# Kernel tuning notes

Measured on AMD Instinct MI355X. Metric: run time of the kernel, lower is better.

Reference implementation:

```python
import jax, jax.numpy as jnp
import numpy as np

D_K = 128
SCALER = np.sqrt(D_K).astype(np.float32)

def setup_inputs() -> dict:
    key = jax.random.key(0)
    kq, kk, kv = jax.random.split(key, 3)
    B, L, D = 16, 2048, D_K
    q = jax.random.normal(kq, (B, L, D), dtype=jnp.float32)
    k = jax.random.normal(kk, (B, L, D), dtype=jnp.float32)
    v = jax.random.normal(kv, (B, L, D), dtype=jnp.float32)
    return {"q": q, "k": k, "v": v}

def reference(q, k, v):
    # score[b, i, j] = q[b, i, :] . k[b, j, :] / sqrt(d_k)
    score = jnp.einsum('bid,bjd->bij', q, k) / SCALER
    attn = jax.nn.softmax(score, axis=-1)
    # output[b, i, :] = sum_j attn[b, i, j] * v[b, j, :]
    return jnp.einsum('bij,bjd->bid', attn, v)
```

## Files before the change

### kernel.cpp

```cpp
#include <hip/hip_runtime.h>
#include <stdint.h>


typedef short bf16x8 __attribute__((ext_vector_type(8)));
typedef float f32x4 __attribute__((ext_vector_type(4)));
typedef unsigned int u32;
typedef unsigned short u16;

#define L_SEQ  2048
#define D_HEAD 128
#define NIT    32
#define TSZ    (16u * 2048u * 128u * 2u)

__device__ __forceinline__ unsigned pk2(float lo, float hi) {
    union { float f; unsigned u; } a, b;
    a.f = lo; b.f = hi;
    return __builtin_amdgcn_perm(b.u + 0x8000u, a.u + 0x8000u, 0x07060302u);
}
__device__ __forceinline__ float ex2(float x) { return __builtin_amdgcn_exp2f(x); }
__device__ __forceinline__ void gl_lds16(const u16* g, u16* l) {
    __builtin_amdgcn_global_load_lds(
        (const __attribute__((address_space(1))) u32*)g,
        (__attribute__((address_space(3))) u32*)l, 16, 0, 0);
}

__global__ __launch_bounds__(256, 4)
void prepass(const float* __restrict__ K, const float* __restrict__ V,
             u16* __restrict__ kb, u16* __restrict__ vt) {
    const int id = blockIdx.x, t = threadIdx.x;
    if (id < 512) {
        const float* src = K + (size_t)id * 64 * 128;
        u16*        dst = kb + (size_t)id * 64 * 128;
        const int r = t >> 2;
        #pragma unroll
        for (int i = 0; i < 4; ++i) {
            int gp = (t & 3) * 4 + i;
            int gs = gp ^ (r & 7);
            const float* s = src + r * 128 + gs * 8;
            float4 x0 = *(const float4*)s, x1 = *(const float4*)(s + 4);
            uint4 w;
            w.x = pk2(x0.x, x0.y); w.y = pk2(x0.z, x0.w);
            w.z = pk2(x1.x, x1.y); w.w = pk2(x1.z, x1.w);
            *(uint4*)(dst + r * 128 + gp * 8) = w;
        }
    } else {
        __shared__ float vl[64 * 132];
        const int bid = id - 512;
        const float* src = V + (size_t)bid * 64 * 128;
        {
            int r = t >> 2, c0 = (t & 3) * 32;
            #pragma unroll
            for (int j = 0; j < 8; ++j)
                *(float4*)(&vl[r * 132 + c0 + j * 4]) =
                    *(const float4*)(src + r * 128 + c0 + j * 4);
        }
        __syncthreads();
        u16* dst = vt + (size_t)bid * 8192;
        const int d = t >> 1;
        #pragma unroll
        for (int i = 0; i < 4; ++i) {
            int gp = (t & 1) * 4 + i;
            int kvb = (gp ^ (d & 7)) * 8;
            float p[8];
            #pragma unroll
            for (int j = 0; j < 8; ++j) p[j] = vl[(kvb + j) * 132 + d];
            uint4 w;
            w.x = pk2(p[0], p[1]); w.y = pk2(p[2], p[3]);
            w.z = pk2(p[4], p[5]); w.w = pk2(p[6], p[7]);
            *(uint4*)(dst + d * 64 + gp * 8) = w;
        }
    }
}

__global__ __launch_bounds__(256, 1)
void attn_fwd(const float* __restrict__ Qg, const u16* __restrict__ kb,
              const u16* __restrict__ vt, float* __restrict__ Og) {
    __shared__ __align__(16) char smem[51200];
    const int tid = threadIdx.x;
    const int wv = tid >> 6, lane = tid & 63;
    const int c = lane & 15, qd = lane >> 4, cx = c & 7;
    const int b = blockIdx.x & 15, qblk = blockIdx.x >> 4;

    const float* Qp = Qg + (size_t)b * L_SEQ * D_HEAD;
    const u16*   Kp = kb + (size_t)b * L_SEQ * D_HEAD;
    const u16*   Vp = vt + (size_t)b * 32 * 8192;
    u16* Kl = (u16*)smem;
    u16* Vl = (u16*)(smem + 16384);
    u16* Pl = (u16*)(smem + 32768) + wv * 2304;

    const int so = wv * 2048 + lane * 8;

    #pragma unroll
    for (int i = 0; i < 4; ++i) {
        gl_lds16(Kp + so + i * 512, Kl + so + i * 512);
        gl_lds16(Vp + so + i * 512, Vl + so + i * 512);
    }

    const float QS = 1.4426950408889634f / 11.313708498984761f;
    bf16x8 qf[2][4];
    #pragma unroll
    for (int s = 0; s < 2; ++s) {
        const float* qrow = Qp + (size_t)(qblk * 128 + wv * 32 + s * 16 + c) * 128 + qd * 8;
        #pragma unroll
        for (int kt = 0; kt < 4; ++kt) {
            float4 x0 = *(const float4*)(qrow + kt * 32);
            float4 x1 = *(const float4*)(qrow + kt * 32 + 4);
            union { unsigned u[4]; bf16x8 v; } tt;
            tt.u[0] = pk2(x0.x * QS, x0.y * QS);
            tt.u[1] = pk2(x0.z * QS, x0.w * QS);
            tt.u[2] = pk2(x1.x * QS, x1.y * QS);
            tt.u[3] = pk2(x1.z * QS, x1.w * QS);
            qf[s][kt] = tt.v;
        }
    }

    f32x4 acc[2][8];
    #pragma unroll
    for (int s = 0; s < 2; ++s)
        #pragma unroll
        for (int dt = 0; dt < 8; ++dt) acc[s][dt] = (f32x4){0.f, 0.f, 0.f, 0.f};
    float lrun[2] = {0.f, 0.f};

    __syncthreads();

    for (int it = 0; it < NIT; ++it) {
        f32x4 st[4][2];
        #pragma unroll
        for (int v = 0; v < 4; ++v) {
            st[v][0] = (f32x4){0.f, 0.f, 0.f, 0.f};
            st[v][1] = (f32x4){0.f, 0.f, 0.f, 0.f};
        }
        #pragma unroll
        for (int kt = 0; kt < 4; ++kt) {
            const int g = ((kt * 4 + qd) ^ cx) * 8;
            #pragma unroll
            for (int v = 0; v < 4; ++v) {
                bf16x8 a = *(const bf16x8*)(Kl + (v * 16 + c) * 128 + g);
                st[v][0] = __builtin_amdgcn_mfma_f32_16x16x32_bf16(a, qf[0][kt], st[v][0], 0, 0, 0);
                st[v][1] = __builtin_amdgcn_mfma_f32_16x16x32_bf16(a, qf[1][kt], st[v][1], 0, 0, 0);
            }
        }
        __syncthreads();

        if (it + 1 < NIT) {
            const u16* kg = Kp + (size_t)(it + 1) * 8192 + so;
            #pragma unroll
            for (int i = 0; i < 4; ++i) gl_lds16(kg + i * 512, Kl + so + i * 512);
        }

        #pragma unroll
        for (int s = 0; s < 2; ++s) {
            float lsum = 0.f;
            #pragma unroll
            for (int v = 0; v < 4; ++v) {
                float p0 = ex2(st[v][s].x), p1 = ex2(st[v][s].y);
                float p2 = ex2(st[v][s].z), p3 = ex2(st[v][s].w);
                lsum += (p0 + p1) + (p2 + p3);
                uint2 w; w.x = pk2(p0, p1); w.y = pk2(p2, p3);
                *(uint2*)(Pl + (s * 16 + c) * 72 + v * 16 + qd * 4) = w;
            }
            lrun[s] += lsum;
        }
        bf16x8 pf[2][2];
        #pragma unroll
        for (int h = 0; h < 2; ++h)
            #pragma unroll
            for (int s = 0; s < 2; ++s)
                pf[h][s] = *(const bf16x8*)(Pl + (s * 16 + c) * 72 + h * 32 + qd * 8);

        #pragma unroll
        for (int dt = 0; dt < 8; ++dt) {
            #pragma unroll
            for (int h = 0; h < 2; ++h) {
                bf16x8 a = *(const bf16x8*)(Vl + (dt * 16 + c) * 64 + ((h * 4 + qd) ^ cx) * 8);
                acc[0][dt] = __builtin_amdgcn_mfma_f32_16x16x32_bf16(a, pf[h][0], acc[0][dt], 0, 0, 0);
                acc[1][dt] = __builtin_amdgcn_mfma_f32_16x16x32_bf16(a, pf[h][1], acc[1][dt], 0, 0, 0);
            }
        }
        __syncthreads();

        if (it + 1 < NIT) {
            const u16* vg = Vp + (size_t)(it + 1) * 8192 + so;
            #pragma unroll
            for (int i = 0; i < 4; ++i) gl_lds16(vg + i * 512, Vl + so + i * 512);
        }
    }

    float inv[2];
    #pragma unroll
    for (int s = 0; s < 2; ++s) {
        float l = lrun[s];
        l += __shfl_xor(l, 16);
        l += __shfl_xor(l, 32);
        inv[s] = 1.0f / l;
    }
    float* Ol = (float*)smem;
    #pragma unroll
    for (int pass = 0; pass < 2; ++pass) {
        if ((wv >> 1) == pass) {
            int rw = (wv & 1) * 32;
            #pragma unroll
            for (int s = 0; s < 2; ++s)
                #pragma unroll
                for (int dt = 0; dt < 8; ++dt) {
                    f32x4 o = acc[s][dt];
                    float4 w = {o.x * inv[s], o.y * inv[s], o.z * inv[s], o.w * inv[s]};
                    *(float4*)(&Ol[(rw + s * 16 + c) * 132 + dt * 16 + qd * 4]) = w;
                }
        }
        __syncthreads();
        #pragma unroll
        for (int i = 0; i < 8; ++i) {
            int idx = i * 256 + tid;
            int row = idx >> 5, c4 = idx & 31;
            float4 val = *(const float4*)(&Ol[row * 132 + c4 * 4]);
            size_t q = (size_t)b * L_SEQ + qblk * 128 + pass * 64 + row;
            *(float4*)(Og + q * D_HEAD + c4 * 4) = val;
        }
        __syncthreads();
    }
}

#define FKST 136
#define FVST 72
#define FPST 72
#define FOST 132
#define FV_OFF  17408
#define FP_OFF  (17408 + 18432)
#define FSMEM   (FP_OFF + 4 * 32 * FPST * 2)

union F4fb { float4 v; float f[4]; };

__global__ __launch_bounds__(256, 1)
void attn_fwd_fb(const float* __restrict__ Qg, const float* __restrict__ Kg,
                 const float* __restrict__ Vg, float* __restrict__ Og) {
    __shared__ __align__(16) char smem[FSMEM];
    unsigned short* Kl = (unsigned short*)(smem);
    unsigned short* Vl = (unsigned short*)(smem + FV_OFF);
    float*          Ol = (float*)smem;

    const int tid  = threadIdx.x;
    const int wv   = tid >> 6;
    const int lane = tid & 63;
    const int c    = lane & 15;
    const int qd   = lane >> 4;
    unsigned short* Pl = (unsigned short*)(smem + FP_OFF) + wv * (32 * FPST);

    const int b  = blockIdx.x & 15;
    const int qb = blockIdx.x >> 4;

    const float* Qb = Qg + (size_t)b * L_SEQ * D_HEAD;
    const float* Kb = Kg + (size_t)b * L_SEQ * D_HEAD;
    const float* Vb = Vg + (size_t)b * L_SEQ * D_HEAD;

    const int krow = tid >> 2, kch = tid & 3;
    const int vcc  = tid & 31, vgk = tid >> 5;

    const float QS = 1.4426950408889634f / 11.313708498984761f;
    bf16x8 qf[2][4];
    #pragma unroll
    for (int s = 0; s < 2; ++s) {
        const float* qrow = Qb + (size_t)(qb * 128 + wv * 32 + s * 16 + c) * D_HEAD + qd * 8;
        #pragma unroll
        for (int kt = 0; kt < 4; ++kt) {
            float4 x0 = *(const float4*)(qrow + kt * 32);
            float4 x1 = *(const float4*)(qrow + kt * 32 + 4);
            union { unsigned u[4]; bf16x8 v; } t;
            t.u[0] = pk2(x0.x * QS, x0.y * QS);
            t.u[1] = pk2(x0.z * QS, x0.w * QS);
            t.u[2] = pk2(x1.x * QS, x1.y * QS);
            t.u[3] = pk2(x1.z * QS, x1.w * QS);
            qf[s][kt] = t.v;
        }
    }

    F4fb kreg[8], vreg[8];
    {
        const float* kp = Kb + (size_t)krow * D_HEAD + kch * 32;
        #pragma unroll
        for (int r = 0; r < 8; ++r) kreg[r].v = *(const float4*)(kp + r * 4);
        const float* vp = Vb + (size_t)(vgk * 8) * D_HEAD + vcc * 4;
        #pragma unroll
        for (int r = 0; r < 8; ++r) vreg[r].v = *(const float4*)(vp + (size_t)r * D_HEAD);
    }

    f32x4 acc[2][8];
    #pragma unroll
    for (int s = 0; s < 2; ++s)
        #pragma unroll
        for (int dt = 0; dt < 8; ++dt) acc[s][dt] = (f32x4){0.f, 0.f, 0.f, 0.f};
    float lrun[2] = {0.f, 0.f};

    for (int it = 0; it < 32; ++it) {
        #pragma unroll
        for (int i = 0; i < 4; ++i) {
            uint4 w;
            w.x = pk2(kreg[2*i].f[0],   kreg[2*i].f[1]);
            w.y = pk2(kreg[2*i].f[2],   kreg[2*i].f[3]);
            w.z = pk2(kreg[2*i+1].f[0], kreg[2*i+1].f[1]);
            w.w = pk2(kreg[2*i+1].f[2], kreg[2*i+1].f[3]);
            *(uint4*)(&Kl[krow * FKST + kch * 32 + i * 8]) = w;
        }
        #pragma unroll
        for (int dd = 0; dd < 4; ++dd) {
            uint4 w;
            w.x = pk2(vreg[0].f[dd], vreg[1].f[dd]);
            w.y = pk2(vreg[2].f[dd], vreg[3].f[dd]);
            w.z = pk2(vreg[4].f[dd], vreg[5].f[dd]);
            w.w = pk2(vreg[6].f[dd], vreg[7].f[dd]);
            *(uint4*)(&Vl[(vcc * 4 + dd) * FVST + vgk * 8]) = w;
        }
        __syncthreads();

        if (it + 1 < 32) {
            const float* kp = Kb + (size_t)((it + 1) * 64 + krow) * D_HEAD + kch * 32;
            #pragma unroll
            for (int r = 0; r < 8; ++r) kreg[r].v = *(const float4*)(kp + r * 4);
            const float* vp = Vb + (size_t)((it + 1) * 64 + vgk * 8) * D_HEAD + vcc * 4;
            #pragma unroll
            for (int r = 0; r < 8; ++r) vreg[r].v = *(const float4*)(vp + (size_t)r * D_HEAD);
        }

        f32x4 st[4][2];
        #pragma unroll
        for (int v = 0; v < 4; ++v) { st[v][0] = (f32x4){0,0,0,0}; st[v][1] = (f32x4){0,0,0,0}; }
        #pragma unroll
        for (int kt = 0; kt < 4; ++kt) {
            #pragma unroll
            for (int v = 0; v < 4; ++v) {
                bf16x8 a = *(const bf16x8*)(&Kl[(v * 16 + c) * FKST + kt * 32 + qd * 8]);
                st[v][0] = __builtin_amdgcn_mfma_f32_16x16x32_bf16(a, qf[0][kt], st[v][0], 0, 0, 0);
                st[v][1] = __builtin_amdgcn_mfma_f32_16x16x32_bf16(a, qf[1][kt], st[v][1], 0, 0, 0);
            }
        }

        #pragma unroll
        for (int s = 0; s < 2; ++s) {
            float lsum = 0.f;
            #pragma unroll
            for (int v = 0; v < 4; ++v) {
                float p0 = ex2(st[v][s].x), p1 = ex2(st[v][s].y);
                float p2 = ex2(st[v][s].z), p3 = ex2(st[v][s].w);
                lsum += (p0 + p1) + (p2 + p3);
                uint2 w; w.x = pk2(p0, p1); w.y = pk2(p2, p3);
                *(uint2*)(&Pl[(s * 16 + c) * FPST + v * 16 + qd * 4]) = w;
            }
            lrun[s] += lsum;
        }
        bf16x8 pf[2][2];
        #pragma unroll
        for (int h = 0; h < 2; ++h)
            #pragma unroll
            for (int s = 0; s < 2; ++s)
                pf[h][s] = *(const bf16x8*)(&Pl[(s * 16 + c) * FPST + h * 32 + qd * 8]);

        #pragma unroll
        for (int dt = 0; dt < 8; ++dt) {
            #pragma unroll
            for (int h = 0; h < 2; ++h) {
                bf16x8 a = *(const bf16x8*)(&Vl[(dt * 16 + c) * FVST + h * 32 + qd * 8]);
                acc[0][dt] = __builtin_amdgcn_mfma_f32_16x16x32_bf16(a, pf[h][0], acc[0][dt], 0, 0, 0);
                acc[1][dt] = __builtin_amdgcn_mfma_f32_16x16x32_bf16(a, pf[h][1], acc[1][dt], 0, 0, 0);
            }
        }
        __syncthreads();
    }

    float inv[2];
    #pragma unroll
    for (int s = 0; s < 2; ++s) {
        float l = lrun[s];
        l += __shfl_xor(l, 16);
        l += __shfl_xor(l, 32);
        inv[s] = 1.0f / l;
    }
    #pragma unroll
    for (int pass = 0; pass < 2; ++pass) {
        if ((wv >> 1) == pass) {
            int rw = (wv & 1) * 32;
            #pragma unroll
            for (int s = 0; s < 2; ++s)
                #pragma unroll
                for (int dt = 0; dt < 8; ++dt) {
                    f32x4 o = acc[s][dt];
                    float4 w = {o.x * inv[s], o.y * inv[s], o.z * inv[s], o.w * inv[s]};
                    *(float4*)(&Ol[(rw + s * 16 + c) * FOST + dt * 16 + qd * 4]) = w;
                }
        }
        __syncthreads();
        #pragma unroll
        for (int i = 0; i < 8; ++i) {
            int idx = i * 256 + tid;
            int row = idx >> 5, c4 = idx & 31;
            float4 val = *(const float4*)(&Ol[row * FOST + c4 * 4]);
            size_t q = (size_t)b * L_SEQ + qb * 128 + pass * 64 + row;
            *(float4*)(Og + q * D_HEAD + c4 * 4) = val;
        }
        __syncthreads();
    }
}

extern "C" void kernel_launch(void* const* d_in, const int* in_sizes, int n_in,
                              void* d_out, int out_size, void* d_ws, size_t ws_size,
                              hipStream_t stream) {
    const float* q = (const float*)d_in[0];
    const float* k = (const float*)d_in[1];
    const float* v = (const float*)d_in[2];
    float* out = (float*)d_out;
    if (ws_size >= (size_t)(2u * TSZ)) {
        u16* kb = (u16*)d_ws;
        u16* vt = (u16*)((char*)d_ws + TSZ);
        prepass<<<dim3(1024), dim3(256), 0, stream>>>(k, v, kb, vt);
        attn_fwd<<<dim3(256), dim3(256), 0, stream>>>(q, kb, vt, out);
    } else {
        attn_fwd_fb<<<dim3(256), dim3(256), 0, stream>>>(q, k, v, out);
    }
}
```

Baseline: 161.7 us.

## Split attention over two KV halves and combine partials in a separate kernel

The attention kernel now launches 512 blocks, each covering half of the key/value sequence for one query block. Unnormalised partial outputs are written as bf16 and row sums as fp32. A new combine kernel adds the two partials, normalises them and writes fp32 output. This targets the under-filled machine (256 blocks on 256 CUs), but adds a kernel launch, extra global traffic for the partials and extra bf16 rounding. Merging partials without a max correction is valid only because the softmax here never subtracts a running max.

```diff
diff --git a/kernel.cpp b/kernel.cpp
--- a/kernel.cpp
+++ b/kernel.cpp
@@ -9,8 +9,11 @@
 
 #define L_SEQ  2048
 #define D_HEAD 128
-#define NIT    32
-#define TSZ    (16u * 2048u * 128u * 2u)
+#define NIT    16
+#define TSZ    8388608u
+#define PART_SZ (512u * 32768u)
+#define LSUM_OFF (2u * TSZ + PART_SZ)
+#define WS_NEED (LSUM_OFF + 512u * 128u * 4u)
 
 __device__ __forceinline__ unsigned pk2(float lo, float hi) {
     union { float f; unsigned u; } a, b;
@@ -18,6 +21,12 @@
     return __builtin_amdgcn_perm(b.u + 0x8000u, a.u + 0x8000u, 0x07060302u);
 }
 __device__ __forceinline__ float ex2(float x) { return __builtin_amdgcn_exp2f(x); }
+__device__ __forceinline__ float bflo(unsigned w) {
+    union { unsigned u; float f; } v; v.u = w << 16; return v.f;
+}
+__device__ __forceinline__ float bfhi(unsigned w) {
+    union { unsigned u; float f; } v; v.u = w & 0xffff0000u; return v.f;
+}
 __device__ __forceinline__ void gl_lds16(const u16* g, u16* l) {
     __builtin_amdgcn_global_load_lds(
         (const __attribute__((address_space(1))) u32*)g,
@@ -72,18 +81,21 @@
     }
 }
 
-__global__ __launch_bounds__(256, 1)
-void attn_fwd(const float* __restrict__ Qg, const u16* __restrict__ kb,
-              const u16* __restrict__ vt, float* __restrict__ Og) {
+__global__ __launch_bounds__(256, 2)
+void attn_split(const float* __restrict__ Qg, const u16* __restrict__ kb,
+                const u16* __restrict__ vt, u16* __restrict__ part,
+                float* __restrict__ lsum) {
     __shared__ __align__(16) char smem[51200];
     const int tid = threadIdx.x;
     const int wv = tid >> 6, lane = tid & 63;
     const int c = lane & 15, qd = lane >> 4, cx = c & 7;
-    const int b = blockIdx.x & 15, qblk = blockIdx.x >> 4;
+    const int bid = blockIdx.x;
+    const int p = bid >> 1, kvh = bid & 1;
+    const int b = p & 15, qblk = p >> 4;
 
     const float* Qp = Qg + (size_t)b * L_SEQ * D_HEAD;
-    const u16*   Kp = kb + (size_t)b * L_SEQ * D_HEAD;
-    const u16*   Vp = vt + (size_t)b * 32 * 8192;
+    const u16*   Kp = kb + (size_t)b * L_SEQ * D_HEAD + (size_t)kvh * 1024 * 128;
+    const u16*   Vp = vt + (size_t)b * 32 * 8192 + (size_t)kvh * 16 * 8192;
     u16* Kl = (u16*)smem;
     u16* Vl = (u16*)(smem + 16384);
     u16* Pl = (u16*)(smem + 32768) + wv * 2304;
@@ -150,16 +162,16 @@
 
         #pragma unroll
         for (int s = 0; s < 2; ++s) {
-            float lsum = 0.f;
+            float lsm = 0.f;
             #pragma unroll
             for (int v = 0; v < 4; ++v) {
                 float p0 = ex2(st[v][s].x), p1 = ex2(st[v][s].y);
                 float p2 = ex2(st[v][s].z), p3 = ex2(st[v][s].w);
-                lsum += (p0 + p1) + (p2 + p3);
+                lsm += (p0 + p1) + (p2 + p3);
                 uint2 w; w.x = pk2(p0, p1); w.y = pk2(p2, p3);
                 *(uint2*)(Pl + (s * 16 + c) * 72 + v * 16 + qd * 4) = w;
             }
-            lrun[s] += lsum;
+            lrun[s] += lsm;
         }
         bf16x8 pf[2][2];
         #pragma unroll
@@ -186,35 +198,71 @@
         }
     }
 
-    float inv[2];
+    float ls[2];
     #pragma unroll
     for (int s = 0; s < 2; ++s) {
         float l = lrun[s];
         l += __shfl_xor(l, 16);
         l += __shfl_xor(l, 32);
-        inv[s] = 1.0f / l;
-    }
-    float* Ol = (float*)smem;
-    #pragma unroll
-    for (int pass = 0; pass < 2; ++pass) {
-        if ((wv >> 1) == pass) {
-            int rw = (wv & 1) * 32;
-            #pragma unroll
-            for (int s = 0; s < 2; ++s)
-                #pragma unroll
-                for (int dt = 0; dt < 8; ++dt) {
-                    f32x4 o = acc[s][dt];
-                    float4 w = {o.x * inv[s], o.y * inv[s], o.z * inv[s], o.w * inv[s]};
-                    *(float4*)(&Ol[(rw + s * 16 + c) * 132 + dt * 16 + qd * 4]) = w;
-                }
-        }
-        __syncthreads();
+        ls[s] = l;
+    }
+    u16* pb = part + (size_t)bid * 16384;
+    #pragma unroll
+    for (int s = 0; s < 2; ++s)
+        #pragma unroll
+        for (int dt = 0; dt < 8; ++dt) {
+            f32x4 o = acc[s][dt];
+            uint2 w; w.x = pk2(o.x, o.y); w.y = pk2(o.z, o.w);
+            *(uint2*)(pb + ((((wv * 2 + s) * 8 + dt) * 64 + lane) << 2)) = w;
+        }
+    if (qd == 0) {
+        lsum[p * 256 + kvh * 128 + wv * 32 + c]      = ls[0];
+        lsum[p * 256 + kvh * 128 + wv * 32 + 16 + c] = ls[1];
+    }
+}
+
+__global__ __launch_bounds__(256, 2)
+void combine(const u16* __restrict__ part, const float* __restrict__ lsum,
+             float* __restrict__ Og) {
+    __shared__ float inv[128];
+    __shared__ __align__(16) float Ol[64 * 132];
+    const int t = threadIdx.x, p = blockIdx.x;
+    const int b = p & 15, qblk = p >> 4;
+    if (t < 128) {
+        float la = lsum[p * 256 + t], lb = lsum[p * 256 + 128 + t];
+        inv[t] = 1.0f / (la + lb);
+    }
+    const uint2* A = (const uint2*)(part + (size_t)(2 * p) * 16384);
+    const uint2* B = (const uint2*)(part + (size_t)(2 * p + 1) * 16384);
+    __syncthreads();
+    #pragma unroll
+    for (int h = 0; h < 2; ++h) {
         #pragma unroll
         for (int i = 0; i < 8; ++i) {
-            int idx = i * 256 + tid;
-            int row = idx >> 5, c4 = idx & 31;
+            int slot = i * 256 + t;
+            int lc = slot >> 6, lane = slot & 63;
+            int gc = h * 32 + lc;
+            int s = (lc >> 3) & 1, dt = lc & 7;
+            int qd = lane >> 4, c = lane & 15;
+            int row = (lc >> 4) * 32 + s * 16 + c;
+            int d0 = dt * 16 + qd * 4;
+            uint2 wa = A[(size_t)gc * 64 + lane];
+            uint2 wb = B[(size_t)gc * 64 + lane];
+            float iv = inv[h * 64 + row];
+            float4 o;
+            o.x = (bflo(wa.x) + bflo(wb.x)) * iv;
+            o.y = (bfhi(wa.x) + bfhi(wb.x)) * iv;
+            o.z = (bflo(wa.y) + bflo(wb.y)) * iv;
+            o.w = (bfhi(wa.y) + bfhi(wb.y)) * iv;
+            *(float4*)(&Ol[row * 132 + d0]) = o;
+        }
+        __syncthreads();
+        #pragma unroll
+        for (int i = 0; i < 8; ++i) {
+            int slot = i * 256 + t;
+            int row = slot >> 5, c4 = slot & 31;
             float4 val = *(const float4*)(&Ol[row * 132 + c4 * 4]);
-            size_t q = (size_t)b * L_SEQ + qblk * 128 + pass * 64 + row;
+            size_t q = (size_t)b * L_SEQ + qblk * 128 + h * 64 + row;
             *(float4*)(Og + q * D_HEAD + c4 * 4) = val;
         }
         __syncthreads();
@@ -336,16 +384,16 @@
 
         #pragma unroll
         for (int s = 0; s < 2; ++s) {
-            float lsum = 0.f;
+            float lsm = 0.f;
             #pragma unroll
             for (int v = 0; v < 4; ++v) {
                 float p0 = ex2(st[v][s].x), p1 = ex2(st[v][s].y);
                 float p2 = ex2(st[v][s].z), p3 = ex2(st[v][s].w);
-                lsum += (p0 + p1) + (p2 + p3);
+                lsm += (p0 + p1) + (p2 + p3);
                 uint2 w; w.x = pk2(p0, p1); w.y = pk2(p2, p3);
                 *(uint2*)(&Pl[(s * 16 + c) * FPST + v * 16 + qd * 4]) = w;
             }
-            lrun[s] += lsum;
+            lrun[s] += lsm;
         }
         bf16x8 pf[2][2];
         #pragma unroll
@@ -407,11 +455,14 @@
     const float* k = (const float*)d_in[1];
     const float* v = (const float*)d_in[2];
     float* out = (float*)d_out;
-    if (ws_size >= (size_t)(2u * TSZ)) {
+    if (ws_size >= (size_t)WS_NEED) {
         u16* kb = (u16*)d_ws;
         u16* vt = (u16*)((char*)d_ws + TSZ);
+        u16* part = (u16*)((char*)d_ws + 2 * (size_t)TSZ);
+        float* ls = (float*)((char*)d_ws + LSUM_OFF);
         prepass<<<dim3(1024), dim3(256), 0, stream>>>(k, v, kb, vt);
-        attn_fwd<<<dim3(256), dim3(256), 0, stream>>>(q, kb, vt, out);
+        attn_split<<<dim3(512), dim3(256), 0, stream>>>(q, kb, vt, part, ls);
+        combine<<<dim3(256), dim3(256), 0, stream>>>(part, ls, out);
     } else {
         attn_fwd_fb<<<dim3(256), dim3(256), 0, stream>>>(q, k, v, out);
     }
```

New measurement: 142.5 us. 1.13x faster.
